# Kernel optimization log

Measured on AMD Instinct MI355X. Metric: run time of the kernel, lower is better.

Reference implementation:

```python
import jax, jax.numpy as jnp
import numpy as np

N, E, H, B = 100000, 1600000, 64, 256
EPS = 1e-5


def ln(x, g, b):
    mu = jnp.mean(x, axis=-1, keepdims=True)
    var = jnp.mean((x - mu) ** 2, axis=-1, keepdims=True)
    return (x - mu) * jax.lax.rsqrt(var + EPS) * g + b


def gelu(x):
    # torch nn.GELU default is exact (erf) gelu
    return jax.nn.gelu(x, approximate=False)


def setup_inputs() -> dict:
    key = jax.random.key(0)
    ks = iter(jax.random.split(key, 64))
    nk = lambda: next(ks)
    s = 0.1
    p = {}
    p["x"] = jax.random.normal(nk(), (N, 2), jnp.float32)
    p["edge_attr"] = jax.random.normal(nk(), (E, 2), jnp.float32)
    # node_embed: Linear(2,H) LN GELU Linear(H,H) LN GELU (dropout = eval no-op)
    p["ne_w1"] = jax.random.normal(nk(), (2, H), jnp.float32) * s
    p["ne_b1"] = jnp.zeros((H,), jnp.float32)
    p["ne_g1"] = jnp.ones((H,), jnp.float32)
    p["ne_be1"] = jnp.zeros((H,), jnp.float32)
    p["ne_w2"] = jax.random.normal(nk(), (H, H), jnp.float32) * s
    p["ne_b2"] = jnp.zeros((H,), jnp.float32)
    p["ne_g2"] = jnp.ones((H,), jnp.float32)
    p["ne_be2"] = jnp.zeros((H,), jnp.float32)
    # 3 TrackConv layers: message MLP Linear(H+2,H)+LN, conv output LN, and outer per-layer LN
    p["conv_w"] = jax.random.normal(nk(), (3, H + 2, H), jnp.float32) * s
    p["conv_b"] = jnp.zeros((3, H), jnp.float32)
    p["conv_mg"] = jnp.ones((3, H), jnp.float32)
    p["conv_mb"] = jnp.zeros((3, H), jnp.float32)
    p["conv_ng"] = jnp.ones((3, H), jnp.float32)
    p["conv_nb"] = jnp.zeros((3, H), jnp.float32)
    p["out_ng"] = jnp.ones((3, H), jnp.float32)
    p["out_nb"] = jnp.zeros((3, H), jnp.float32)
    # head MLP: Linear(H,H)+LN+ReLU, Linear(H,H//2)+LN+ReLU, Linear(H//2,1)
    p["m_w1"] = jax.random.normal(nk(), (H, H), jnp.float32) * s
    p["m_b1"] = jnp.zeros((H,), jnp.float32)
    p["m_g1"] = jnp.ones((H,), jnp.float32)
    p["m_be1"] = jnp.zeros((H,), jnp.float32)
    p["m_w2"] = jax.random.normal(nk(), (H, H // 2), jnp.float32) * s
    p["m_b2"] = jnp.zeros((H // 2,), jnp.float32)
    p["m_g2"] = jnp.ones((H // 2,), jnp.float32)
    p["m_be2"] = jnp.zeros((H // 2,), jnp.float32)
    p["m_w3"] = jax.random.normal(nk(), (H // 2, 1), jnp.float32) * s
    p["m_b3"] = jnp.zeros((1,), jnp.float32)
    p["edge_index"] = jax.random.randint(nk(), (2, E), 0, N, dtype=jnp.int32)
    p["batch"] = jnp.sort(jax.random.randint(nk(), (N,), 0, B, dtype=jnp.int32))
    return p


def reference(x, edge_attr,
              ne_w1, ne_b1, ne_g1, ne_be1, ne_w2, ne_b2, ne_g2, ne_be2,
              conv_w, conv_b, conv_mg, conv_mb, conv_ng, conv_nb, out_ng, out_nb,
              m_w1, m_b1, m_g1, m_be1, m_w2, m_b2, m_g2, m_be2, m_w3, m_b3,
              edge_index, batch):
    # node embedding (dropout in eval = identity)
    h = gelu(ln(x @ ne_w1 + ne_b1, ne_g1, ne_be1))
    h = gelu(ln(h @ ne_w2 + ne_b2, ne_g2, ne_be2))
    src, dst = edge_index[0], edge_index[1]  # PyG: message from src (x_j), aggregate at dst
    deg = jax.ops.segment_sum(jnp.ones((E,), h.dtype), dst, num_segments=N)
    deg = jnp.maximum(deg, 1.0)[:, None]
    for l in range(3):
        msg_in = jnp.concatenate([h[src], edge_attr], axis=-1)  # [E, H+2]
        msg = gelu(ln(msg_in @ conv_w[l] + conv_b[l], conv_mg[l], conv_mb[l]))  # [E, H]
        agg = jax.ops.segment_sum(msg, dst, num_segments=N) / deg  # mean aggregate
        conv_out = ln(agg + h, conv_ng[l], conv_nb[l])  # TrackConv: norm(out + residual)
        h = h + ln(conv_out, out_ng[l], out_nb[l])  # outer norm + residual
    # global mean pool over graphs
    cnt = jnp.maximum(jax.ops.segment_sum(jnp.ones((N,), h.dtype), batch, num_segments=B), 1.0)[:, None]
    g = jax.ops.segment_sum(h, batch, num_segments=B) / cnt  # [B, H]
    g = jax.nn.relu(ln(g @ m_w1 + m_b1, m_g1, m_be1))
    g = jax.nn.relu(ln(g @ m_w2 + m_b2, m_g2, m_be2))
    return g @ m_w3 + m_b3  # [B, 1]
```

## Files before the change

### kernel.cpp

```cpp
#include <hip/hip_runtime.h>
#include <math.h>


typedef __attribute__((ext_vector_type(8))) short bfrag;
typedef __attribute__((ext_vector_type(4))) float ffrag;

template <int CTRL>
__device__ __forceinline__ float dpp_mov(float v) {
  return __int_as_float(
      __builtin_amdgcn_update_dpp(0, __float_as_int(v), CTRL, 0xF, 0xF, true));
}

__device__ __forceinline__ float rsum16(float v) {
  v += dpp_mov<0x128>(v);
  v += dpp_mov<0x124>(v);
  v += dpp_mov<0x122>(v);
  v += dpp_mov<0x121>(v);
  return v;
}

__device__ __forceinline__ float wave_sum64(float v) {
  v = rsum16(v);
  v += __shfl_xor(v, 16, 64);
  v += __shfl_xor(v, 32, 64);
  return v;
}

__device__ __forceinline__ float ln_apply(float t, float g, float b) {
  float s1 = wave_sum64(t);
  float s2 = wave_sum64(t * t);
  float mu = s1 * 0.015625f;
  float var = fmaf(-mu, mu, s2 * 0.015625f);
  return (t - mu) * rsqrtf(var + 1e-5f) * g + b;
}

__device__ __forceinline__ float erf_fast(float x) {
  float ax = fabsf(x);
  float p = fmaf(fmaf(fmaf(fmaf(0.078108f, ax, 0.000972f), ax, 0.230389f),
                      ax, 0.278393f), ax, 1.0f);
  p = p * p;
  p = p * p;
  float r = __builtin_amdgcn_rcpf(p);
  return copysignf(1.0f - r, x);
}

__device__ __forceinline__ float gelu_exact(float v) {
  float half = 0.5f * v;
  return fmaf(half, erf_fast(v * 0.70710678118654752440f), half);
}

__device__ __forceinline__ float lane_bcast(float v, int k) {
  return __uint_as_float(__builtin_amdgcn_readlane(__float_as_uint(v), k));
}

__device__ __forceinline__ short f2bf(float f) {
  union { float f; unsigned u; } v; v.f = f;
  unsigned r = v.u + 0x7fffu + ((v.u >> 16) & 1u);
  return (short)(r >> 16);
}

__global__ __launch_bounds__(256) void k_init(
    const float* __restrict__ x,
    const float* __restrict__ w1, const float* __restrict__ b1,
    const float* __restrict__ g1, const float* __restrict__ be1,
    const float* __restrict__ w2, const float* __restrict__ b2,
    const float* __restrict__ g2, const float* __restrict__ be2,
    const float* __restrict__ conv_w, ushort* __restrict__ wt,
    const int* __restrict__ ei, int* __restrict__ csr,
    float* __restrict__ h, ushort* __restrict__ hb,
    int n_nodes, int ne, int oHist, int oEmb, int embWaves) {
  const int bid = blockIdx.x;
  const int tid = threadIdx.x;
  if (bid < oHist) {
    const int i = bid * 256 + tid;
    const int k = i % 96, f = (i / 96) % 64, l = i / (96 * 64);
    const float v = (k < 66) ? conv_w[(size_t)l * 66 * 64 + k * 64 + f] : 0.0f;
    wt[i] = (ushort)f2bf(v);
    return;
  }
  if (bid < oEmb) {
    const int i = (bid - oHist) * 256 + tid;
    if (i < ne) atomicAdd(&csr[ei[ne + i]], 1);
    return;
  }
  const int lane = tid & 63;
  const int wid = ((bid - oEmb) * 256 + tid) >> 6;
  const int nw = embWaves;
  float wc[64];
#pragma unroll
  for (int k = 0; k < 64; k++) wc[k] = w2[k * 64 + lane];
  const float w1a = w1[lane], w1b = w1[64 + lane];
  const float vb1 = b1[lane], vg1 = g1[lane], vbe1 = be1[lane];
  const float vb2 = b2[lane], vg2 = g2[lane], vbe2 = be2[lane];
  for (int n = wid; n < n_nodes; n += nw) {
    const float x0 = x[2 * n], x1 = x[2 * n + 1];
    float t = fmaf(x0, w1a, fmaf(x1, w1b, vb1));
    t = gelu_exact(ln_apply(t, vg1, vbe1));
    float a0 = vb2, a1 = 0.f, a2 = 0.f, a3 = 0.f;
#pragma unroll
    for (int k = 0; k < 64; k += 4) {
      a0 = fmaf(lane_bcast(t, k + 0), wc[k + 0], a0);
      a1 = fmaf(lane_bcast(t, k + 1), wc[k + 1], a1);
      a2 = fmaf(lane_bcast(t, k + 2), wc[k + 2], a2);
      a3 = fmaf(lane_bcast(t, k + 3), wc[k + 3], a3);
    }
    float acc = (a0 + a1) + (a2 + a3);
    acc = gelu_exact(ln_apply(acc, vg2, vbe2));
    h[n * 64 + lane] = acc;
    hb[n * 64 + lane] = (ushort)f2bf(acc);
  }
}

__global__ __launch_bounds__(1024) void k_scan_fast(int* __restrict__ buf, int n) {
  __shared__ int wsum[16];
  const int tid = threadIdx.x, lane = tid & 63, w = tid >> 6;
  const int chunk = (((n + 1023) / 1024) + 3) & ~3;
  const int a = min(tid * chunk, n), b = min(a + chunk, n);
  const bool full = (a + chunk <= n);
  int s = 0;
  if (full) {
    const int4* p4 = (const int4*)(buf + a);
#pragma unroll 4
    for (int i = 0; i < chunk / 4; i++) {
      int4 v = p4[i];
      s += v.x + v.y + v.z + v.w;
    }
  } else {
    for (int i = a; i < b; i++) s += buf[i];
  }
  int inc = s;
#pragma unroll
  for (int sh = 1; sh < 64; sh <<= 1) {
    int t = __shfl_up(inc, sh, 64);
    if (lane >= sh) inc += t;
  }
  if (lane == 63) wsum[w] = inc;
  __syncthreads();
  int wb = 0;
  for (int j = 0; j < w; j++) wb += wsum[j];
  int excl = wb + inc - s;
  if (full) {
    int4* p4 = (int4*)(buf + a);
#pragma unroll 4
    for (int i = 0; i < chunk / 4; i++) {
      int4 v = p4[i];
      int4 o;
      o.x = excl; excl += v.x;
      o.y = excl; excl += v.y;
      o.z = excl; excl += v.z;
      o.w = excl; excl += v.w;
      p4[i] = o;
    }
  } else {
    for (int i = a; i < b; i++) { int v = buf[i]; buf[i] = excl; excl += v; }
  }
}

__global__ void k_scatter(const int* __restrict__ ei, const float* __restrict__ ea,
                          int* __restrict__ cursor, int4* __restrict__ edata, int ne) {
  int i = blockIdx.x * blockDim.x + threadIdx.x;
  if (i < ne) {
    const int d = ei[ne + i];
    const int s = ei[i];
    const float2 eav = *(const float2*)(ea + 2 * (size_t)i);
    const unsigned pk = (unsigned)(ushort)f2bf(eav.x) |
                        ((unsigned)(ushort)f2bf(eav.y) << 16);
    const int pos = atomicAdd(&cursor[d], 1);
    edata[pos] = make_int4(s, (int)pk, d, 0);
  }
}

__global__ __launch_bounds__(256, 3) void k_edge_packed(
    const ushort* __restrict__ hb_in, float* __restrict__ agg,
    const int4* __restrict__ edata, const ushort* __restrict__ wt,
    const float* __restrict__ bias, const float* __restrict__ mg,
    const float* __restrict__ mb, int nchunks, int ne) {
  __shared__ __align__(16) ushort lwt[64 * 96];
  {
    const uint4* s = (const uint4*)wt;
    uint4* d = (uint4*)lwt;
    for (int i = threadIdx.x; i < 768; i += 256) d[i] = s[i];
  }
  __syncthreads();

  const int lane = threadIdx.x & 63;
  const int grp = lane >> 4, col = lane & 15;
  const int wid = (blockIdx.x * blockDim.x + threadIdx.x) >> 6;
  const int nw = (gridDim.x * blockDim.x) >> 6;

  float vb[4], vg[4], vbb[4];
#pragma unroll
  for (int t = 0; t < 4; t++) {
    const int f = t * 16 + col;
    vb[t] = bias[f]; vg[t] = mg[f]; vbb[t] = mb[f];
  }

  int c = wid;
  if (c >= nchunks) return;
  int4 e = edata[min(16 * c + col, ne - 1)];
  {
    const ushort* hp = hb_in + (size_t)e.x * 64 + grp * 8;
  }
  const ushort* hp0 = hb_in + (size_t)e.x * 64 + grp * 8;
  bfrag A0 = *(const bfrag*)(hp0);
  bfrag A1 = *(const bfrag*)(hp0 + 32);

  for (;;) {
    const int rem = min(16, ne - 16 * c);
    const int cn = c + nw;
    const bool more = cn < nchunks;
    const int nslot = more ? min(16 * cn + col, ne - 1) : min(16 * c + col, ne - 1);
    const int4 en = edata[nslot];

    bfrag A2 = {0, 0, 0, 0, 0, 0, 0, 0};
    if (grp == 0) {
      A2[0] = (short)(e.y & 0xffff);
      A2[1] = (short)((unsigned)e.y >> 16);
    }

    ffrag acc[4];
#pragma unroll
    for (int t = 0; t < 4; t++) { ffrag cc = {vb[t], vb[t], vb[t], vb[t]}; acc[t] = cc; }
#pragma unroll
    for (int t = 0; t < 4; t++) {
      const bfrag B = *(const bfrag*)(lwt + (t * 16 + col) * 96 + grp * 8);
      acc[t] = __builtin_amdgcn_mfma_f32_16x16x32_bf16(A0, B, acc[t], 0, 0, 0);
    }
#pragma unroll
    for (int t = 0; t < 4; t++) {
      const bfrag B = *(const bfrag*)(lwt + (t * 16 + col) * 96 + 32 + grp * 8);
      acc[t] = __builtin_amdgcn_mfma_f32_16x16x32_bf16(A1, B, acc[t], 0, 0, 0);
    }
#pragma unroll
    for (int t = 0; t < 4; t++) {
      const bfrag B = *(const bfrag*)(lwt + (t * 16 + col) * 96 + 64 + grp * 8);
      acc[t] = __builtin_amdgcn_mfma_f32_16x16x32_bf16(A2, B, acc[t], 0, 0, 0);
    }

    const ushort* hq = hb_in + (size_t)en.x * 64 + grp * 8;
    const bfrag N0 = *(const bfrag*)(hq);
    const bfrag N1 = *(const bfrag*)(hq + 32);

    float sx[4], sq[4];
#pragma unroll
    for (int r = 0; r < 4; r++) {
      float s = (acc[0][r] + acc[1][r]) + (acc[2][r] + acc[3][r]);
      float q = fmaf(acc[0][r], acc[0][r], fmaf(acc[1][r], acc[1][r],
                fmaf(acc[2][r], acc[2][r], acc[3][r] * acc[3][r])));
      sx[r] = s; sq[r] = q;
    }
#pragma unroll
    for (int r = 0; r < 4; r++) sx[r] = rsum16(sx[r]);
#pragma unroll
    for (int r = 0; r < 4; r++) sq[r] = rsum16(sq[r]);
    float iv[4], mi[4];
#pragma unroll
    for (int r = 0; r < 4; r++) {
      const float mu = sx[r] * 0.015625f;
      const float var = fmaf(-mu, mu, sq[r] * 0.015625f);
      iv[r] = rsqrtf(var + 1e-5f);
      mi[r] = -mu * iv[r];
    }

#pragma unroll
    for (int t = 0; t < 4; t++) {
#pragma unroll
      for (int r = 0; r < 4; r++) {
        const float z = fmaf(acc[t][r], iv[r], mi[r]);
        acc[t][r] = gelu_exact(fmaf(z, vg[t], vbb[t]));
      }
    }

    const int prev = __shfl_up(e.z, 1, 64);
    const unsigned long long bal = __ballot((col > 0) && (e.z != prev));
    const unsigned bm = (unsigned)bal & 0xFFFEu;

    int s0 = 0;
    while (s0 < rem) {
      const unsigned rest = bm >> (s0 + 1);
      int s1 = rest ? (s0 + 1 + __builtin_ctz(rest)) : 16;
      if (s1 > rem) s1 = rem;
      const int dseg = __builtin_amdgcn_readlane(e.z, s0);
#pragma unroll
      for (int t = 0; t < 4; t++) {
        float rs = 0.f;
#pragma unroll
        for (int r = 0; r < 4; r++) {
          const int row = grp * 4 + r;
          const float w = (row >= s0 && row < s1) ? 1.0f : 0.0f;
          rs = fmaf(acc[t][r], w, rs);
        }
        rs += __shfl_xor(rs, 16, 64);
        rs += __shfl_xor(rs, 32, 64);
        if (lane < 16)
          atomicAdd(&agg[(size_t)dseg * 64 + t * 16 + lane], rs);
      }
      s0 = s1;
    }

    if (!more) break;
    c = cn; e = en; A0 = N0; A1 = N1;
  }
}

__global__ void k_node_update(float* __restrict__ h, ushort* __restrict__ hb,
                              float* __restrict__ agg, const int* __restrict__ ends,
                              const float* __restrict__ ng, const float* __restrict__ nb,
                              const float* __restrict__ og, const float* __restrict__ ob,
                              int n_nodes, int writeHb) {
  const int lane = threadIdx.x & 63;
  const int n = (blockIdx.x * blockDim.x + threadIdx.x) >> 6;
  if (n >= n_nodes) return;
  int start, end;
  if (n == 0) { start = 0; end = ends[0]; }
  else { const int2 se = *(const int2*)(ends + n - 1); start = se.x; end = se.y; }
  const float dg = fmaxf((float)(end - start), 1.0f);
  const float hv = h[(size_t)n * 64 + lane];
  const float a = agg[(size_t)n * 64 + lane] / dg + hv;
  if (writeHb) agg[(size_t)n * 64 + lane] = 0.0f;
  const float c = ln_apply(a, ng[lane], nb[lane]);
  const float o = ln_apply(c, og[lane], ob[lane]);
  const float outv = hv + o;
  h[(size_t)n * 64 + lane] = outv;
  if (writeHb) hb[(size_t)n * 64 + lane] = (ushort)f2bf(outv);
}

__global__ void k_pool_seg(const float* __restrict__ h, const int* __restrict__ batch,
                           float* __restrict__ g, float* __restrict__ cnt,
                           int n_nodes, int chunk) {
  const int lane = threadIdx.x & 63;
  const int wid = (blockIdx.x * blockDim.x + threadIdx.x) >> 6;
  const int n0 = wid * chunk;
  if (n0 >= n_nodes) return;
  const int n1 = min(n0 + chunk, n_nodes);
  int cur = batch[n0], c = 0;
  float acc = 0.f;
  for (int n = n0; n < n1; n++) {
    const int b = batch[n];
    if (b != cur) {
      atomicAdd(&g[(size_t)cur * 64 + lane], acc);
      if (lane == 0) atomicAdd(&cnt[cur], (float)c);
      acc = 0.f; c = 0; cur = b;
    }
    acc += h[(size_t)n * 64 + lane];
    c++;
  }
  atomicAdd(&g[(size_t)cur * 64 + lane], acc);
  if (lane == 0) atomicAdd(&cnt[cur], (float)c);
}

__global__ void k_head(const float* __restrict__ g, const float* __restrict__ cnt,
                       const float* __restrict__ w1, const float* __restrict__ b1,
                       const float* __restrict__ g1, const float* __restrict__ be1,
                       const float* __restrict__ w2, const float* __restrict__ b2,
                       const float* __restrict__ g2, const float* __restrict__ be2,
                       const float* __restrict__ w3, const float* __restrict__ b3,
                       float* __restrict__ out, int nb_) {
  const int lane = threadIdx.x & 63;
  const int row = (blockIdx.x * blockDim.x + threadIdx.x) >> 6;
  if (row >= nb_) return;
  const float c = fmaxf(cnt[row], 1.0f);
  const float gv = g[row * 64 + lane] / c;
  float a0 = b1[lane], a1 = 0.f, a2 = 0.f, a3 = 0.f;
#pragma unroll
  for (int k = 0; k < 64; k += 4) {
    a0 = fmaf(lane_bcast(gv, k + 0), w1[(k + 0) * 64 + lane], a0);
    a1 = fmaf(lane_bcast(gv, k + 1), w1[(k + 1) * 64 + lane], a1);
    a2 = fmaf(lane_bcast(gv, k + 2), w1[(k + 2) * 64 + lane], a2);
    a3 = fmaf(lane_bcast(gv, k + 3), w1[(k + 3) * 64 + lane], a3);
  }
  float t = (a0 + a1) + (a2 + a3);
  t = fmaxf(ln_apply(t, g1[lane], be1[lane]), 0.0f);

  const int j = lane & 31;
  float c0 = b2[j], c1 = 0.f, c2 = 0.f, c3 = 0.f;
#pragma unroll
  for (int k = 0; k < 64; k += 4) {
    c0 = fmaf(lane_bcast(t, k + 0), w2[(k + 0) * 32 + j], c0);
    c1 = fmaf(lane_bcast(t, k + 1), w2[(k + 1) * 32 + j], c1);
    c2 = fmaf(lane_bcast(t, k + 2), w2[(k + 2) * 32 + j], c2);
    c3 = fmaf(lane_bcast(t, k + 3), w2[(k + 3) * 32 + j], c3);
  }
  float t2 = (c0 + c1) + (c2 + c3);
  t2 = fmaxf(ln_apply(t2, g2[j], be2[j]), 0.0f);
  const float p = t2 * w3[j];
  const float s = wave_sum64(p) * 0.5f;
  if (lane == 0) out[row] = s + b3[0];
}

extern "C" void kernel_launch(void* const* d_in, const int* in_sizes, int n_in,
                              void* d_out, int out_size, void* d_ws, size_t ws_size,
                              hipStream_t stream) {
  const float* x      = (const float*)d_in[0];
  const float* ea     = (const float*)d_in[1];
  const float* ne_w1  = (const float*)d_in[2];
  const float* ne_b1  = (const float*)d_in[3];
  const float* ne_g1  = (const float*)d_in[4];
  const float* ne_be1 = (const float*)d_in[5];
  const float* ne_w2  = (const float*)d_in[6];
  const float* ne_b2  = (const float*)d_in[7];
  const float* ne_g2  = (const float*)d_in[8];
  const float* ne_be2 = (const float*)d_in[9];
  const float* conv_w = (const float*)d_in[10];
  const float* conv_b = (const float*)d_in[11];
  const float* conv_mg= (const float*)d_in[12];
  const float* conv_mb= (const float*)d_in[13];
  const float* conv_ng= (const float*)d_in[14];
  const float* conv_nb= (const float*)d_in[15];
  const float* out_ng = (const float*)d_in[16];
  const float* out_nb = (const float*)d_in[17];
  const float* m_w1   = (const float*)d_in[18];
  const float* m_b1   = (const float*)d_in[19];
  const float* m_g1   = (const float*)d_in[20];
  const float* m_be1  = (const float*)d_in[21];
  const float* m_w2   = (const float*)d_in[22];
  const float* m_b2   = (const float*)d_in[23];
  const float* m_g2   = (const float*)d_in[24];
  const float* m_be2  = (const float*)d_in[25];
  const float* m_w3   = (const float*)d_in[26];
  const float* m_b3   = (const float*)d_in[27];
  const int*   eidx   = (const int*)d_in[28];
  const int*   batch  = (const int*)d_in[29];
  float* outp = (float*)d_out;

  const int NN = in_sizes[29];
  const int NE = in_sizes[1] / 2;
  const int NB = out_size;
  const int NCH = (NE + 15) / 16;

  char* wsb = (char*)d_ws;
  float*  h    = (float*)wsb;
  ushort* hb   = (ushort*)(h + (size_t)NN * 64);
  int4*   edata= (int4*)((char*)hb + ((size_t)NN * 128 + 15) / 16 * 16);
  ushort* wt   = (ushort*)(edata + NE);
  float*  gbuf = (float*)(wt + 3 * 64 * 96);
  float*  cnt  = gbuf + (size_t)NB * 64;
  int*    csr  = (int*)(cnt + NB);
  float*  agg  = (float*)((char*)(csr + NN) +
                          (((size_t)(uintptr_t)(csr + NN) & 15) ? 16 - ((size_t)(uintptr_t)(csr + NN) & 15) : 0));

  const dim3 blk(256);

  const size_t zbytes = (char*)(agg + (size_t)NN * 64) - (char*)gbuf;
  hipMemsetAsync(gbuf, 0, zbytes, stream);

  const int nPrep = (3 * 64 * 96) / 256;
  const int nHist = (NE + 255) / 256;
  const int oHist = nPrep, oEmb = nPrep + nHist;
  const int embBlocks = 2048;
  k_init<<<oEmb + embBlocks, blk, 0, stream>>>(
      x, ne_w1, ne_b1, ne_g1, ne_be1, ne_w2, ne_b2, ne_g2, ne_be2,
      conv_w, wt, eidx, csr, h, hb, NN, NE, oHist, oEmb, embBlocks * 4);

  k_scan_fast<<<1, 1024, 0, stream>>>(csr, NN);
  k_scatter<<<(NE + 255) / 256, blk, 0, stream>>>(eidx, ea, csr, edata, NE);

  for (int l = 0; l < 3; l++) {
    k_edge_packed<<<4096, blk, 0, stream>>>(
        hb, agg, edata, wt + (size_t)l * 64 * 96,
        conv_b + l * 64, conv_mg + l * 64, conv_mb + l * 64, NCH, NE);
    k_node_update<<<(NN * 64 + 255) / 256, blk, 0, stream>>>(
        h, hb, agg, csr, conv_ng + l * 64, conv_nb + l * 64,
        out_ng + l * 64, out_nb + l * 64, NN, (l < 2) ? 1 : 0);
  }

  {
    const int chunk = 32;
    const int nwaves = (NN + chunk - 1) / chunk;
    const int nblocks = (nwaves * 64 + 255) / 256;
    k_pool_seg<<<nblocks, blk, 0, stream>>>(h, batch, gbuf, cnt, NN, chunk);
  }
  k_head<<<(NB + 3) / 4, blk, 0, stream>>>(gbuf, cnt, m_w1, m_b1, m_g1, m_be1,
                                           m_w2, m_b2, m_g2, m_be2, m_w3, m_b3,
                                           outp, NB);
}
```

Before: 766.2 us.

## Move node embedding into scatter kernel and use nontemporal edge-data stores

Node-embedding work moves out of the histogram/init kernel and into a combined kernel with the CSR scatter. The embedding blocks then run alongside the atomic-heavy scatter instead of the histogram, which shortens the preprocessing kernel that precedes the single-block scan. Edge-data writes become nontemporal stores to limit cache pollution. This rebalances which stage hides the embedding compute, but the scatter kernel now carries more register pressure from the embedding path.

```diff
diff --git a/kernel.cpp b/kernel.cpp
--- a/kernel.cpp
+++ b/kernel.cpp
@@ -4,6 +4,7 @@
 
 typedef __attribute__((ext_vector_type(8))) short bfrag;
 typedef __attribute__((ext_vector_type(4))) float ffrag;
+typedef __attribute__((ext_vector_type(4))) int iv4;
 
 template <int CTRL>
 __device__ __forceinline__ float dpp_mov(float v) {
@@ -59,16 +60,10 @@
   return (short)(r >> 16);
 }
 
-__global__ __launch_bounds__(256) void k_init(
-    const float* __restrict__ x,
-    const float* __restrict__ w1, const float* __restrict__ b1,
-    const float* __restrict__ g1, const float* __restrict__ be1,
-    const float* __restrict__ w2, const float* __restrict__ b2,
-    const float* __restrict__ g2, const float* __restrict__ be2,
+__global__ __launch_bounds__(256) void k_init1(
     const float* __restrict__ conv_w, ushort* __restrict__ wt,
     const int* __restrict__ ei, int* __restrict__ csr,
-    float* __restrict__ h, ushort* __restrict__ hb,
-    int n_nodes, int ne, int oHist, int oEmb, int embWaves) {
+    int ne, int oHist) {
   const int bid = blockIdx.x;
   const int tid = threadIdx.x;
   if (bid < oHist) {
@@ -78,37 +73,8 @@
     wt[i] = (ushort)f2bf(v);
     return;
   }
-  if (bid < oEmb) {
-    const int i = (bid - oHist) * 256 + tid;
-    if (i < ne) atomicAdd(&csr[ei[ne + i]], 1);
-    return;
-  }
-  const int lane = tid & 63;
-  const int wid = ((bid - oEmb) * 256 + tid) >> 6;
-  const int nw = embWaves;
-  float wc[64];
-#pragma unroll
-  for (int k = 0; k < 64; k++) wc[k] = w2[k * 64 + lane];
-  const float w1a = w1[lane], w1b = w1[64 + lane];
-  const float vb1 = b1[lane], vg1 = g1[lane], vbe1 = be1[lane];
-  const float vb2 = b2[lane], vg2 = g2[lane], vbe2 = be2[lane];
-  for (int n = wid; n < n_nodes; n += nw) {
-    const float x0 = x[2 * n], x1 = x[2 * n + 1];
-    float t = fmaf(x0, w1a, fmaf(x1, w1b, vb1));
-    t = gelu_exact(ln_apply(t, vg1, vbe1));
-    float a0 = vb2, a1 = 0.f, a2 = 0.f, a3 = 0.f;
-#pragma unroll
-    for (int k = 0; k < 64; k += 4) {
-      a0 = fmaf(lane_bcast(t, k + 0), wc[k + 0], a0);
-      a1 = fmaf(lane_bcast(t, k + 1), wc[k + 1], a1);
-      a2 = fmaf(lane_bcast(t, k + 2), wc[k + 2], a2);
-      a3 = fmaf(lane_bcast(t, k + 3), wc[k + 3], a3);
-    }
-    float acc = (a0 + a1) + (a2 + a3);
-    acc = gelu_exact(ln_apply(acc, vg2, vbe2));
-    h[n * 64 + lane] = acc;
-    hb[n * 64 + lane] = (ushort)f2bf(acc);
-  }
+  const int i = (bid - oHist) * 256 + tid;
+  if (i < ne) atomicAdd(&csr[ei[ne + i]], 1);
 }
 
 __global__ __launch_bounds__(1024) void k_scan_fast(int* __restrict__ buf, int n) {
@@ -156,17 +122,57 @@
   }
 }
 
-__global__ void k_scatter(const int* __restrict__ ei, const float* __restrict__ ea,
-                          int* __restrict__ cursor, int4* __restrict__ edata, int ne) {
-  int i = blockIdx.x * blockDim.x + threadIdx.x;
-  if (i < ne) {
-    const int d = ei[ne + i];
-    const int s = ei[i];
-    const float2 eav = *(const float2*)(ea + 2 * (size_t)i);
-    const unsigned pk = (unsigned)(ushort)f2bf(eav.x) |
-                        ((unsigned)(ushort)f2bf(eav.y) << 16);
-    const int pos = atomicAdd(&cursor[d], 1);
-    edata[pos] = make_int4(s, (int)pk, d, 0);
+__global__ __launch_bounds__(256) void k_combo(
+    const int* __restrict__ ei, const float* __restrict__ ea,
+    int* __restrict__ cursor, int4* __restrict__ edata,
+    const float* __restrict__ x,
+    const float* __restrict__ w1, const float* __restrict__ b1,
+    const float* __restrict__ g1, const float* __restrict__ be1,
+    const float* __restrict__ w2, const float* __restrict__ b2,
+    const float* __restrict__ g2, const float* __restrict__ be2,
+    float* __restrict__ h, ushort* __restrict__ hb,
+    int n_nodes, int ne, int oEmb, int embWaves) {
+  const int bid = blockIdx.x;
+  const int tid = threadIdx.x;
+  if (bid < oEmb) {
+    const int i = bid * 256 + tid;
+    if (i < ne) {
+      const int d = ei[ne + i];
+      const int s = ei[i];
+      const float2 eav = *(const float2*)(ea + 2 * (size_t)i);
+      const unsigned pk = (unsigned)(ushort)f2bf(eav.x) |
+                          ((unsigned)(ushort)f2bf(eav.y) << 16);
+      const int pos = atomicAdd(&cursor[d], 1);
+      iv4 v = {s, (int)pk, d, 0};
+      __builtin_nontemporal_store(v, (iv4*)(edata + pos));
+    }
+    return;
+  }
+  const int lane = tid & 63;
+  const int wid = ((bid - oEmb) * 256 + tid) >> 6;
+  const int nw = embWaves;
+  float wc[64];
+#pragma unroll
+  for (int k = 0; k < 64; k++) wc[k] = w2[k * 64 + lane];
+  const float w1a = w1[lane], w1b = w1[64 + lane];
+  const float vb1 = b1[lane], vg1 = g1[lane], vbe1 = be1[lane];
+  const float vb2 = b2[lane], vg2 = g2[lane], vbe2 = be2[lane];
+  for (int n = wid; n < n_nodes; n += nw) {
+    const float x0 = x[2 * n], x1 = x[2 * n + 1];
+    float t = fmaf(x0, w1a, fmaf(x1, w1b, vb1));
+    t = gelu_exact(ln_apply(t, vg1, vbe1));
+    float a0 = vb2, a1 = 0.f, a2 = 0.f, a3 = 0.f;
+#pragma unroll
+    for (int k = 0; k < 64; k += 4) {
+      a0 = fmaf(lane_bcast(t, k + 0), wc[k + 0], a0);
+      a1 = fmaf(lane_bcast(t, k + 1), wc[k + 1], a1);
+      a2 = fmaf(lane_bcast(t, k + 2), wc[k + 2], a2);
+      a3 = fmaf(lane_bcast(t, k + 3), wc[k + 3], a3);
+    }
+    float acc = (a0 + a1) + (a2 + a3);
+    acc = gelu_exact(ln_apply(acc, vg2, vbe2));
+    h[n * 64 + lane] = acc;
+    hb[n * 64 + lane] = (ushort)f2bf(acc);
   }
 }
 
@@ -198,9 +204,6 @@
   int c = wid;
   if (c >= nchunks) return;
   int4 e = edata[min(16 * c + col, ne - 1)];
-  {
-    const ushort* hp = hb_in + (size_t)e.x * 64 + grp * 8;
-  }
   const ushort* hp0 = hb_in + (size_t)e.x * 64 + grp * 8;
   bfrag A0 = *(const bfrag*)(hp0);
   bfrag A1 = *(const bfrag*)(hp0 + 32);
@@ -446,14 +449,16 @@
 
   const int nPrep = (3 * 64 * 96) / 256;
   const int nHist = (NE + 255) / 256;
-  const int oHist = nPrep, oEmb = nPrep + nHist;
+  k_init1<<<nPrep + nHist, blk, 0, stream>>>(conv_w, wt, eidx, csr, NE, nPrep);
+
+  k_scan_fast<<<1, 1024, 0, stream>>>(csr, NN);
+
+  const int nScat = (NE + 255) / 256;
   const int embBlocks = 2048;
-  k_init<<<oEmb + embBlocks, blk, 0, stream>>>(
-      x, ne_w1, ne_b1, ne_g1, ne_be1, ne_w2, ne_b2, ne_g2, ne_be2,
-      conv_w, wt, eidx, csr, h, hb, NN, NE, oHist, oEmb, embBlocks * 4);
-
-  k_scan_fast<<<1, 1024, 0, stream>>>(csr, NN);
-  k_scatter<<<(NE + 255) / 256, blk, 0, stream>>>(eidx, ea, csr, edata, NE);
+  k_combo<<<nScat + embBlocks, blk, 0, stream>>>(
+      eidx, ea, csr, edata, x,
+      ne_w1, ne_b1, ne_g1, ne_be1, ne_w2, ne_b2, ne_g2, ne_be2,
+      h, hb, NN, NE, nScat, embBlocks * 4);
 
   for (int l = 0; l < 3; l++) {
     k_edge_packed<<<4096, blk, 0, stream>>>(
```

After: 761.4 us. No clear change (-0.6%).
